# Optimization experiments

Measured on AMD Instinct MI355X. Metric: run time of the kernel, lower is better.

Reference implementation:

```python
import jax, jax.numpy as jnp
import numpy as np

T = 4      # num_step (also LSTM num_layers)
R = 64     # num_relation (= LSTM hidden size)
E = 1024   # num_entity
B = 128    # batch
IN = R + 2 * E  # LSTM input size


def _lstm_layer(x_seq, Wih, Whh, bih, bhh):
    # x_seq: [T, B, In]; torch gate order i, f, g, o
    Bsz = x_seq.shape[1]
    H = Whh.shape[1]
    pre = jnp.einsum('tbi,gi->tbg', x_seq, Wih) + bih + bhh  # [T,B,4H]

    def step(carry, z):
        h, c = carry
        z = z + h @ Whh.T
        i, f, g, o = jnp.split(z, 4, axis=-1)
        i, f, o = jax.nn.sigmoid(i), jax.nn.sigmoid(f), jax.nn.sigmoid(o)
        c = f * c + i * jnp.tanh(g)
        h = o * jnp.tanh(c)
        return (h, c), h

    init = (jnp.zeros((Bsz, H), x_seq.dtype), jnp.zeros((Bsz, H), x_seq.dtype))
    _, hs = jax.lax.scan(step, init, pre)
    return hs  # [T, B, H]


def setup_inputs() -> dict:
    key = jax.random.key(0)
    ks = jax.random.split(key, 12)
    s = 0.05
    inp = {
        'x': jax.random.uniform(ks[0], (B, IN), dtype=jnp.float32),
        'kb': jax.random.uniform(ks[1], (R, E, E), dtype=jnp.float32) * 0.01,
        # LSTM layer 0 (input dim IN)
        'Wih0': jax.random.normal(ks[2], (4 * R, IN), dtype=jnp.float32) * s,
        'Whh0': jax.random.normal(ks[3], (4 * R, R), dtype=jnp.float32) * s,
        'bih0': jnp.zeros((4 * R,), jnp.float32),
        'bhh0': jnp.zeros((4 * R,), jnp.float32),
        # LSTM layers 1..T-1 (input dim R)
        'Wih': jax.random.normal(ks[4], (T - 1, 4 * R, R), dtype=jnp.float32) * s,
        'Whh': jax.random.normal(ks[5], (T - 1, 4 * R, R), dtype=jnp.float32) * s,
        'bih': jnp.zeros((T - 1, 4 * R), jnp.float32),
        'bhh': jnp.zeros((T - 1, 4 * R), jnp.float32),
    }
    return inp


def reference(x, kb, Wih0, Whh0, bih0, bhh0, Wih, Whh, bih, bhh):
    # input to LSTM: x repeated T times -> [T, B, IN]
    seq = jnp.broadcast_to(x[None], (T,) + x.shape)
    hs = _lstm_layer(seq, Wih0, Whh0, bih0, bhh0)
    for l in range(T - 1):  # small fixed layer count
        hs = _lstm_layer(hs, Wih[l], Whh[l], bih[l], bhh[l])
    h = jax.nn.softmax(hs, axis=-1)  # [T, B, R] (first softmax)

    mem = [x[:, R:R + E]]  # memory[0] = head entity vector, [B, E]
    for i in range(T):
        h2 = jax.nn.softmax(h[i], axis=-1)  # double softmax, faithful to source
        # causal memory attention over steps k <= i
        att = jax.nn.softmax(jnp.einsum('kbr,br->bk', h[:i + 1], h[i]), axis=-1)  # [B, i+1]
        prev = jnp.einsum('bk,kbe->be', att, jnp.stack(mem))  # [B, E]
        # per-relation operator application: sum_r h2[b,r] * KB[r] @ prev[b]
        tmp = jnp.einsum('ref,bf->bre', kb, prev)  # [B, R, E]
        mem.append(jnp.einsum('br,bre->be', h2, tmp))

    tail = x[:, R + E:R + 2 * E]  # [B, E]
    score = jax.nn.sigmoid(-jnp.einsum('be,be->b', mem[-1], tail))[:, None]  # [B, 1]
    return score
```

## Files before the change

### kernel.cpp

```cpp
#include <hip/hip_runtime.h>
#include <cstdint>
#include <cstddef>

#define B_ 128
#define E_ 1024
#define R_ 64
#define T_ 4
#define IN_ 2112
#define G_ 256

typedef __attribute__((ext_vector_type(4))) float f32x4;
typedef __attribute__((ext_vector_type(8))) __bf16 bf16x8;

__device__ __forceinline__ unsigned short f2bf(float f) {
  unsigned int u = __float_as_uint(f);
  u += 0x7fffu + ((u >> 16) & 1u);
  return (unsigned short)(u >> 16);
}
__device__ __forceinline__ unsigned int pack2(float lo, float hi) {
  return (unsigned int)f2bf(lo) | ((unsigned int)f2bf(hi) << 16);
}
__device__ __forceinline__ float wred_sum(float v) {
#pragma unroll
  for (int m = 32; m > 0; m >>= 1) v += __shfl_xor(v, m, 64);
  return v;
}
__device__ __forceinline__ float wred_max(float v) {
#pragma unroll
  for (int m = 32; m > 0; m >>= 1) v = fmaxf(v, __shfl_xor(v, m, 64));
  return v;
}
__device__ __forceinline__ float sigmoidf_(float x) { return 1.f / (1.f + expf(-x)); }

__device__ __forceinline__ void gload_lds16(const void* g, void* l) {
  __builtin_amdgcn_global_load_lds(
      (const __attribute__((address_space(1))) unsigned int*)g,
      (__attribute__((address_space(3))) unsigned int*)l, 16, 0, 0);
}

__global__ __launch_bounds__(256, 2) void head_kernel(
    const float* __restrict__ x, const float* __restrict__ kb,
    const float* __restrict__ Wih0, const float* __restrict__ Whh0,
    const float* __restrict__ bih0, const float* __restrict__ bhh0,
    const float* __restrict__ Wih, const float* __restrict__ Whh,
    const float* __restrict__ bih, const float* __restrict__ bhh,
    unsigned short* __restrict__ kb_bf,
    float* __restrict__ h2_out, float* __restrict__ att_out,
    unsigned short* __restrict__ prev_bf) {
  const int tid = threadIdx.x;

  if (blockIdx.x >= 128) {
    const size_t base = (size_t)(blockIdx.x - 128) * 8192;
#pragma unroll
    for (int c = 0; c < 4; c++) {
      size_t o = base + (size_t)c * 2048 + (size_t)tid * 8;
      float4 v0 = *(const float4*)(kb + o);
      float4 v1 = *(const float4*)(kb + o + 4);
      uint4 u;
      u.x = pack2(v0.x, v0.y); u.y = pack2(v0.z, v0.w);
      u.z = pack2(v1.x, v1.y); u.w = pack2(v1.z, v1.w);
      *(uint4*)(kb_bf + o) = u;
    }
    return;
  }

  __shared__ __align__(16) float xrow[IN_];
  __shared__ __align__(16) float hbuf[R_];
  __shared__ __align__(16) float zbuf[2][G_];
  __shared__ __align__(16) float hs_out[T_][R_];
  __shared__ __align__(16) float hmat[T_][R_];

  const int b = blockIdx.x;
  const int lane = tid & 63, wv = tid >> 6;
  const int s = tid & 63;

  for (int l = tid; l < IN_; l += 256) xrow[l] = x[b * IN_ + l];
  __syncthreads();
  float p0;
  {
    float4 acc4 = {0.f, 0.f, 0.f, 0.f};
    const float4* wr4 = (const float4*)(Wih0 + (size_t)tid * IN_);
    const float4* xr4 = (const float4*)xrow;
#pragma unroll 8
    for (int j = 0; j < IN_ / 4; j++) {
      float4 w = wr4[j];
      float4 xv = xr4[j];
      acc4.x += xv.x * w.x; acc4.y += xv.y * w.y;
      acc4.z += xv.z * w.z; acc4.w += xv.w * w.w;
    }
    p0 = bih0[tid] + bhh0[tid] + ((acc4.x + acc4.y) + (acc4.z + acc4.w));
  }

  float4 w4[16];
  float pret[T_];

  auto scan = [&]() {
    __syncthreads();
    hbuf[s] = 0.f;
    float creg = 0.f;
#pragma unroll
    for (int t = 0; t < T_; t++) {
      float z = pret[t];
#pragma unroll
      for (int q = 0; q < 16; q++) {
        float4 hv = *(const float4*)(&hbuf[q * 4]);
        z += hv.x * w4[q].x + hv.y * w4[q].y + hv.z * w4[q].z + hv.w * w4[q].w;
      }
      zbuf[t & 1][tid] = z;
      __syncthreads();
      float iv = sigmoidf_(zbuf[t & 1][s]);
      float fv = sigmoidf_(zbuf[t & 1][R_ + s]);
      float gv = tanhf(zbuf[t & 1][2 * R_ + s]);
      float ov = sigmoidf_(zbuf[t & 1][3 * R_ + s]);
      creg = fv * creg + iv * gv;
      float h = ov * tanhf(creg);
      hbuf[s] = h;
      hs_out[t][s] = h;
    }
  };

#pragma unroll
  for (int t = 0; t < T_; t++) pret[t] = p0;
#pragma unroll
  for (int q = 0; q < 16; q++)
    w4[q] = *(const float4*)(Whh0 + (size_t)tid * R_ + q * 4);
  scan();

  for (int l = 0; l < T_ - 1; l++) {
#pragma unroll
    for (int q = 0; q < 16; q++)
      w4[q] = *(const float4*)(Wih + ((size_t)l * G_ + tid) * R_ + q * 4);
    const float bsum = bih[l * G_ + tid] + bhh[l * G_ + tid];
#pragma unroll
    for (int t = 0; t < T_; t++) {
      float p = bsum;
#pragma unroll
      for (int q = 0; q < 16; q++) {
        float4 hv = *(const float4*)(&hs_out[t][q * 4]);
        p += hv.x * w4[q].x + hv.y * w4[q].y + hv.z * w4[q].z + hv.w * w4[q].w;
      }
      pret[t] = p;
    }
#pragma unroll
    for (int q = 0; q < 16; q++)
      w4[q] = *(const float4*)(Whh + ((size_t)l * G_ + tid) * R_ + q * 4);
    scan();
  }

  {
    float v = hs_out[wv][lane];
    float mx = wred_max(v);
    float ev = expf(v - mx);
    float sm = wred_sum(ev);
    float hval = ev / sm;
    hmat[wv][lane] = hval;
    float mx2 = wred_max(hval);
    float e2 = expf(hval - mx2);
    float s2 = wred_sum(e2);
    h2_out[(wv * B_ + b) * R_ + lane] = e2 / s2;
    __syncthreads();
    float dots[T_];
    for (int k = 0; k <= wv; k++)
      dots[k] = wred_sum(hmat[k][lane] * hmat[wv][lane]);
    if (lane == 0) {
      float mx3 = dots[0];
      for (int k = 1; k <= wv; k++) mx3 = fmaxf(mx3, dots[k]);
      float ss = 0.f, es[T_];
      for (int k = 0; k <= wv; k++) { es[k] = expf(dots[k] - mx3); ss += es[k]; }
      for (int k = 0; k <= wv; k++) att_out[(wv * B_ + b) * 4 + k] = es[k] / ss;
    }
  }

  for (int l = tid; l < E_; l += 256)
    prev_bf[b * E_ + l] = f2bf(xrow[R_ + l]);
}

__global__ __launch_bounds__(256) void gemm_bf_kernel(
    const unsigned short* __restrict__ Abf,
    const unsigned short* __restrict__ Kbf,
    float* __restrict__ part) {
  __shared__ unsigned short As[2][128 * 32];
  __shared__ unsigned short Bs[2][128 * 32];
  const int tid = threadIdx.x, wv = tid >> 6, lane = tid & 63;
  const int et = blockIdx.x, r = blockIdx.y;
  const int wm = (wv & 1) * 64, wn = (wv >> 1) * 64;
  const int fr = lane & 15, koff = (lane >> 4) * 8;

  const int srow = wv * 32 + (lane >> 2);
  const int scol = (lane & 3) * 8;
  const unsigned short* agp = Abf + (size_t)srow * 1024 + scol;
  const unsigned short* bgp = Kbf + (size_t)r * 1048576 + (size_t)(et * 128 + srow) * 1024 + scol;

  f32x4 acc[4][4];
#pragma unroll
  for (int mt = 0; mt < 4; mt++)
#pragma unroll
    for (int nt = 0; nt < 4; nt++)
#pragma unroll
      for (int q = 0; q < 4; q++) acc[mt][nt][q] = 0.f;

  auto stage = [&](int buf, int kk) {
    gload_lds16(agp + kk * 32,             As[buf] + wv * 1024);
    gload_lds16(agp + kk * 32 + 16 * 1024, As[buf] + wv * 1024 + 512);
    gload_lds16(bgp + kk * 32,             Bs[buf] + wv * 1024);
    gload_lds16(bgp + kk * 32 + 16 * 1024, Bs[buf] + wv * 1024 + 512);
  };

  stage(0, 0);
  __syncthreads();
  int cur = 0;
  for (int kk = 0; kk < 32; kk++) {
    if (kk < 31) stage(cur ^ 1, kk + 1);
    bf16x8 af[4], bfr[4];
#pragma unroll
    for (int mt = 0; mt < 4; mt++)
      af[mt] = *(const bf16x8*)(As[cur] + (wm + mt * 16 + fr) * 32 + koff);
#pragma unroll
    for (int nt = 0; nt < 4; nt++)
      bfr[nt] = *(const bf16x8*)(Bs[cur] + (wn + nt * 16 + fr) * 32 + koff);
#pragma unroll
    for (int mt = 0; mt < 4; mt++)
#pragma unroll
      for (int nt = 0; nt < 4; nt++)
        acc[mt][nt] = __builtin_amdgcn_mfma_f32_16x16x32_bf16(af[mt], bfr[nt], acc[mt][nt], 0, 0, 0);
    __syncthreads();
    cur ^= 1;
  }
  const int crow = (lane >> 4) * 4;
  float* pout = part + (size_t)r * 131072;
#pragma unroll
  for (int mt = 0; mt < 4; mt++)
#pragma unroll
    for (int nt = 0; nt < 4; nt++)
#pragma unroll
      for (int q = 0; q < 4; q++)
        pout[(wm + mt * 16 + crow + q) * 1024 + et * 128 + wn + nt * 16 + fr] = acc[mt][nt][q];
}

__global__ __launch_bounds__(256) void mid_kernel(
    const float* __restrict__ part, const float* __restrict__ h2,
    const float* __restrict__ att, const float* __restrict__ x,
    float* __restrict__ mem, unsigned short* __restrict__ prev_bf, int it) {
  const int idx = blockIdx.x * 256 + threadIdx.x;
  const int b = idx >> 10, e = idx & 1023;
  const float* h2row = h2 + (it * B_ + b) * R_;
  const float* pp = part + idx;
  float s = 0.f;
#pragma unroll 8
  for (int rr = 0; rr < 64; rr++) s += h2row[rr] * pp[(size_t)rr * 131072];
  mem[it * 131072 + idx] = s;
  if (it < 3) {
    const float* arow = att + ((it + 1) * B_ + b) * 4;
    float acc = arow[0] * x[b * IN_ + R_ + e];
    for (int k = 1; k <= it; k++) acc += arow[k] * mem[(k - 1) * 131072 + idx];
    acc += arow[it + 1] * s;
    prev_bf[idx] = f2bf(acc);
  }
}

__global__ __launch_bounds__(256) void prep_fp32_kernel(
    const float* __restrict__ x, const float* __restrict__ att,
    const float* __restrict__ mem, float* __restrict__ prev,
    float* __restrict__ newmem, int it) {
  const int idx = blockIdx.x * 256 + threadIdx.x;
  const int b = idx >> 10, e = idx & 1023;
  const float* arow = att + (it * B_ + b) * 4;
  float acc = arow[0] * x[b * IN_ + R_ + e];
  for (int k = 1; k <= it; k++)
    acc += arow[k] * mem[(k - 1) * (B_ * E_) + b * E_ + e];
  prev[idx] = acc;
  newmem[idx] = 0.f;
}

__global__ __launch_bounds__(256) void gemm_fp32_kernel(
    const float* __restrict__ prev, const float* __restrict__ h2,
    const float* __restrict__ kb, float* __restrict__ out) {
  __shared__ unsigned short As[128 * 40];
  __shared__ unsigned short Bs[128 * 40];
  __shared__ float h2s[128];
  const int tid = threadIdx.x;
  const int et = blockIdx.x;
  const int r = blockIdx.y;
  if (tid < 128) h2s[tid] = h2[tid * 64 + r];
  __syncthreads();
  const int row = tid >> 1;
  const int c0 = (tid & 1) * 16;
  const float hsc = h2s[row];
  const float* aptr = prev + row * 1024 + c0;
  const float* bptr = kb + (size_t)r * (1024u * 1024u) + (size_t)(et * 128 + row) * 1024 + c0;
  unsigned short* adst = As + row * 40 + c0;
  unsigned short* bdst = Bs + row * 40 + c0;
  const int wv = tid >> 6, lane = tid & 63;
  const int wm = (wv & 1) * 64, wn = (wv >> 1) * 64;
  const int fr = lane & 15, koff = (lane >> 4) * 8;
  f32x4 acc[4][4];
#pragma unroll
  for (int mt = 0; mt < 4; mt++)
#pragma unroll
    for (int nt = 0; nt < 4; nt++)
#pragma unroll
      for (int q = 0; q < 4; q++) acc[mt][nt][q] = 0.f;
  for (int kk = 0; kk < 32; kk++) {
    const float4 a0 = *(const float4*)(aptr + kk * 32);
    const float4 a1 = *(const float4*)(aptr + kk * 32 + 4);
    const float4 a2 = *(const float4*)(aptr + kk * 32 + 8);
    const float4 a3 = *(const float4*)(aptr + kk * 32 + 12);
    const float4 b0 = *(const float4*)(bptr + kk * 32);
    const float4 b1 = *(const float4*)(bptr + kk * 32 + 4);
    const float4 b2 = *(const float4*)(bptr + kk * 32 + 8);
    const float4 b3 = *(const float4*)(bptr + kk * 32 + 12);
    __syncthreads();
    uint4 u;
    u.x = pack2(a0.x * hsc, a0.y * hsc); u.y = pack2(a0.z * hsc, a0.w * hsc);
    u.z = pack2(a1.x * hsc, a1.y * hsc); u.w = pack2(a1.z * hsc, a1.w * hsc);
    *(uint4*)adst = u;
    u.x = pack2(a2.x * hsc, a2.y * hsc); u.y = pack2(a2.z * hsc, a2.w * hsc);
    u.z = pack2(a3.x * hsc, a3.y * hsc); u.w = pack2(a3.z * hsc, a3.w * hsc);
    *(uint4*)(adst + 8) = u;
    u.x = pack2(b0.x, b0.y); u.y = pack2(b0.z, b0.w);
    u.z = pack2(b1.x, b1.y); u.w = pack2(b1.z, b1.w);
    *(uint4*)bdst = u;
    u.x = pack2(b2.x, b2.y); u.y = pack2(b2.z, b2.w);
    u.z = pack2(b3.x, b3.y); u.w = pack2(b3.z, b3.w);
    *(uint4*)(bdst + 8) = u;
    __syncthreads();
    bf16x8 af[4], bfr[4];
#pragma unroll
    for (int mt = 0; mt < 4; mt++)
      af[mt] = *(const bf16x8*)(As + (wm + mt * 16 + fr) * 40 + koff);
#pragma unroll
    for (int nt = 0; nt < 4; nt++)
      bfr[nt] = *(const bf16x8*)(Bs + (wn + nt * 16 + fr) * 40 + koff);
#pragma unroll
    for (int mt = 0; mt < 4; mt++)
#pragma unroll
      for (int nt = 0; nt < 4; nt++)
        acc[mt][nt] = __builtin_amdgcn_mfma_f32_16x16x32_bf16(af[mt], bfr[nt], acc[mt][nt], 0, 0, 0);
  }
  const int crow = (lane >> 4) * 4;
  const int ccol = et * 128 + fr;
#pragma unroll
  for (int mt = 0; mt < 4; mt++)
#pragma unroll
    for (int nt = 0; nt < 4; nt++)
#pragma unroll
      for (int q = 0; q < 4; q++)
        atomicAdd(&out[(wm + mt * 16 + crow + q) * 1024 + ccol + wn + nt * 16], acc[mt][nt][q]);
}

__global__ __launch_bounds__(256) void score_kernel(
    const float* __restrict__ x, const float* __restrict__ mem4,
    float* __restrict__ out) {
  __shared__ float red[4];
  const int b = blockIdx.x, tid = threadIdx.x;
  float s = 0.f;
  for (int e = tid; e < E_; e += 256)
    s += mem4[b * E_ + e] * x[b * IN_ + R_ + E_ + e];
  s = wred_sum(s);
  if ((tid & 63) == 0) red[tid >> 6] = s;
  __syncthreads();
  if (tid == 0) {
    float t = red[0] + red[1] + red[2] + red[3];
    out[b] = 1.f / (1.f + expf(t));
  }
}

extern "C" void kernel_launch(void* const* d_in, const int* in_sizes, int n_in,
                              void* d_out, int out_size, void* d_ws, size_t ws_size,
                              hipStream_t stream) {
  const float* x    = (const float*)d_in[0];
  const float* kb   = (const float*)d_in[1];
  const float* Wih0 = (const float*)d_in[2];
  const float* Whh0 = (const float*)d_in[3];
  const float* bih0 = (const float*)d_in[4];
  const float* bhh0 = (const float*)d_in[5];
  const float* Wih  = (const float*)d_in[6];
  const float* Whh  = (const float*)d_in[7];
  const float* bih  = (const float*)d_in[8];
  const float* bhh  = (const float*)d_in[9];

  float* ws    = (float*)d_ws;
  float* h2    = ws;
  float* att   = ws + 32768;
  float* mem   = ws + 34816;
  float* prevb = ws + 559104;
  float* part  = ws + 690176;
  float* kbbf  = ws + 9078784;
  const size_t need_big = (size_t)(9078784 + 33554432) * sizeof(float);
  const bool big = ws_size >= need_big;

  if (big) {
    head_kernel<<<8320, 256, 0, stream>>>(x, kb, Wih0, Whh0, bih0, bhh0,
                                          Wih, Whh, bih, bhh,
                                          (unsigned short*)kbbf, h2, att,
                                          (unsigned short*)prevb);
    for (int i = 0; i < 4; i++) {
      gemm_bf_kernel<<<dim3(8, 64), 256, 0, stream>>>(
          (const unsigned short*)prevb, (const unsigned short*)kbbf, part);
      mid_kernel<<<512, 256, 0, stream>>>(part, h2, att, x, mem,
                                          (unsigned short*)prevb, i);
    }
  } else {
    head_kernel<<<128, 256, 0, stream>>>(x, kb, Wih0, Whh0, bih0, bhh0,
                                         Wih, Whh, bih, bhh,
                                         (unsigned short*)prevb , h2, att,
                                         (unsigned short*)prevb);
    for (int i = 0; i < 4; i++) {
      float* newmem = mem + i * (B_ * E_);
      prep_fp32_kernel<<<512, 256, 0, stream>>>(x, att, mem, prevb, newmem, i);
      gemm_fp32_kernel<<<dim3(8, 64), 256, 0, stream>>>(prevb, h2 + i * (B_ * R_), kb, newmem);
    }
  }
  score_kernel<<<128, 256, 0, stream>>>(x, mem + 3 * (B_ * E_), (float*)d_out);
}
```

Before: 620.8 us.

## Load GEMM fragments directly from global memory into registers, dropping LDS staging

The bf16 GEMM kernel no longer stages A and B tiles through double-buffered LDS with global_load_lds and barriers. Each wave now loads its MFMA fragments straight from global memory into registers, using a two-step register double buffer to overlap loads with MFMAs. This removes the LDS traffic and the per-iteration __syncthreads. In exchange, waves sharing the same A/B rows load them redundantly from global/L2, and the 16-byte row-strided reads coalesce less well.

```diff
diff --git a/kernel.cpp b/kernel.cpp
--- a/kernel.cpp
+++ b/kernel.cpp
@@ -31,12 +31,6 @@
   return v;
 }
 __device__ __forceinline__ float sigmoidf_(float x) { return 1.f / (1.f + expf(-x)); }
-
-__device__ __forceinline__ void gload_lds16(const void* g, void* l) {
-  __builtin_amdgcn_global_load_lds(
-      (const __attribute__((address_space(1))) unsigned int*)g,
-      (__attribute__((address_space(3))) unsigned int*)l, 16, 0, 0);
-}
 
 __global__ __launch_bounds__(256, 2) void head_kernel(
     const float* __restrict__ x, const float* __restrict__ kb,
@@ -179,17 +173,20 @@
     const unsigned short* __restrict__ Abf,
     const unsigned short* __restrict__ Kbf,
     float* __restrict__ part) {
-  __shared__ unsigned short As[2][128 * 32];
-  __shared__ unsigned short Bs[2][128 * 32];
   const int tid = threadIdx.x, wv = tid >> 6, lane = tid & 63;
   const int et = blockIdx.x, r = blockIdx.y;
   const int wm = (wv & 1) * 64, wn = (wv >> 1) * 64;
   const int fr = lane & 15, koff = (lane >> 4) * 8;
 
-  const int srow = wv * 32 + (lane >> 2);
-  const int scol = (lane & 3) * 8;
-  const unsigned short* agp = Abf + (size_t)srow * 1024 + scol;
-  const unsigned short* bgp = Kbf + (size_t)r * 1048576 + (size_t)(et * 128 + srow) * 1024 + scol;
+  const unsigned short* ap[4];
+  const unsigned short* bp[4];
+#pragma unroll
+  for (int mt = 0; mt < 4; mt++)
+    ap[mt] = Abf + (size_t)(wm + mt * 16 + fr) * 1024 + koff;
+#pragma unroll
+  for (int nt = 0; nt < 4; nt++)
+    bp[nt] = Kbf + (size_t)r * 1048576 +
+             (size_t)(et * 128 + wn + nt * 16 + fr) * 1024 + koff;
 
   f32x4 acc[4][4];
 #pragma unroll
@@ -199,33 +196,38 @@
 #pragma unroll
       for (int q = 0; q < 4; q++) acc[mt][nt][q] = 0.f;
 
-  auto stage = [&](int buf, int kk) {
-    gload_lds16(agp + kk * 32,             As[buf] + wv * 1024);
-    gload_lds16(agp + kk * 32 + 16 * 1024, As[buf] + wv * 1024 + 512);
-    gload_lds16(bgp + kk * 32,             Bs[buf] + wv * 1024);
-    gload_lds16(bgp + kk * 32 + 16 * 1024, Bs[buf] + wv * 1024 + 512);
-  };
-
-  stage(0, 0);
-  __syncthreads();
-  int cur = 0;
-  for (int kk = 0; kk < 32; kk++) {
-    if (kk < 31) stage(cur ^ 1, kk + 1);
-    bf16x8 af[4], bfr[4];
+  bf16x8 a0[4], b0[4], a1[4], b1[4];
+#pragma unroll
+  for (int i = 0; i < 4; i++) {
+    a0[i] = *(const bf16x8*)(ap[i]);
+    b0[i] = *(const bf16x8*)(bp[i]);
+  }
+
+  for (int kk = 0; kk < 32; kk += 2) {
+#pragma unroll
+    for (int i = 0; i < 4; i++) {
+      a1[i] = *(const bf16x8*)(ap[i] + (kk + 1) * 32);
+      b1[i] = *(const bf16x8*)(bp[i] + (kk + 1) * 32);
+    }
 #pragma unroll
     for (int mt = 0; mt < 4; mt++)
-      af[mt] = *(const bf16x8*)(As[cur] + (wm + mt * 16 + fr) * 32 + koff);
-#pragma unroll
-    for (int nt = 0; nt < 4; nt++)
-      bfr[nt] = *(const bf16x8*)(Bs[cur] + (wn + nt * 16 + fr) * 32 + koff);
+#pragma unroll
+      for (int nt = 0; nt < 4; nt++)
+        acc[mt][nt] = __builtin_amdgcn_mfma_f32_16x16x32_bf16(a0[mt], b0[nt], acc[mt][nt], 0, 0, 0);
+    if (kk + 2 < 32) {
+#pragma unroll
+      for (int i = 0; i < 4; i++) {
+        a0[i] = *(const bf16x8*)(ap[i] + (kk + 2) * 32);
+        b0[i] = *(const bf16x8*)(bp[i] + (kk + 2) * 32);
+      }
+    }
 #pragma unroll
     for (int mt = 0; mt < 4; mt++)
 #pragma unroll
       for (int nt = 0; nt < 4; nt++)
-        acc[mt][nt] = __builtin_amdgcn_mfma_f32_16x16x32_bf16(af[mt], bfr[nt], acc[mt][nt], 0, 0, 0);
-    __syncthreads();
-    cur ^= 1;
-  }
+        acc[mt][nt] = __builtin_amdgcn_mfma_f32_16x16x32_bf16(a1[mt], b1[nt], acc[mt][nt], 0, 0, 0);
+  }
+
   const int crow = (lane >> 4) * 4;
   float* pout = part + (size_t)r * 131072;
 #pragma unroll
```

Result: slower. 748.0 us (+20.5%).
